# Kernel optimization log

Measured on AMD Instinct MI355X. Metric: run time of the kernel, lower is better.

## Reference

```python
import jax, jax.numpy as jnp
import numpy as np
from jax import lax

DIM = 512
DIM_KEY = 128


def _conv3x3_s2(x, w):
    # x: [N, C, H, W], w: [O, I, 3, 3]; stride-2, VALID (matches nn.Conv2d(dim, dim, 3, stride=2))
    return lax.conv_general_dilated(
        x, w, window_strides=(2, 2), padding='VALID',
        dimension_numbers=('NCHW', 'OIHW', 'NCHW'))


def setup_inputs() -> dict:
    key = jax.random.key(0)
    k1, k2, k3, k4, k5 = jax.random.split(key, 5)
    b, k, n, H, W = 8, 5, 5, 41, 41
    return {
        'img_query': jax.random.normal(k1, (b, DIM, H, W), dtype=jnp.float32),
        'img_supports': jax.random.normal(k2, (b, k, n, DIM, H, W), dtype=jnp.float32),
        'w_qk': jax.random.normal(k3, (DIM_KEY, DIM), dtype=jnp.float32) * 0.02,
        'w_v': jax.random.normal(k4, (DIM_KEY, DIM), dtype=jnp.float32) * 0.02,
        'w_ms': jax.random.normal(k5, (DIM, DIM, 3, 3), dtype=jnp.float32) * 0.02,
    }


def reference(img_query, img_supports, w_qk, w_v, w_ms):
    scale = DIM_KEY ** -0.5
    b, k, n = img_supports.shape[:3]

    # backbone `model` treated as identity; then multi-scale extracter (3x3 s2 conv)
    query_repr = _conv3x3_s2(img_query, w_ms)              # [b, c, h, w]
    h, w = query_repr.shape[-2:]
    supports = img_supports.reshape(b * k * n, DIM, *img_supports.shape[-2:])
    supports_repr = _conv3x3_s2(supports, w_ms)            # [bkn, c, h, w]

    # 1x1 convs as channel contractions
    query_q = jnp.einsum('bchw,dc->bdhw', query_repr, w_qk)
    query_v = jnp.einsum('bchw,dc->bdhw', query_repr, w_v)
    supports_k = jnp.einsum('schw,dc->sdhw', supports_repr, w_qk).reshape(b, k, n, DIM_KEY, h, w)
    supports_v = jnp.einsum('schw,dc->sdhw', supports_repr, w_v).reshape(b, k, n, DIM_KEY, h, w)

    # many-to-many cross attention over (n, i, j)
    sim = jnp.einsum('bchw,bkncij->bkhwnij', query_q, supports_k) * scale
    attn = jax.nn.softmax(sim.reshape(b, k, h, w, n * h * w), axis=-1)
    attn = attn.reshape(b, k, h, w, n, h, w)
    out = jnp.einsum('bkhwnij,bkncij->bkchw', attn, supports_v)

    out = out.reshape(b, k, -1)                     # [b, k, c*h*w]
    qv = query_v.reshape(b, 1, -1)                  # [b, 1, c*h*w]
    euclidean_dist = jnp.sum((qv - out) ** 2, axis=-1) / (h * w)
    return -euclidean_dist                          # [b, k]
```

## Files before the change

kernel.cpp:

```cpp
#include <hip/hip_runtime.h>

#define DIMC   512
#define HWIN   1681
#define WIN_   41
#define HWOUT  400
#define COUT   256
#define KD     4608
#define NIMG   208
#define NPAIR  40
#define NJ     2000

typedef __bf16 bf16;
typedef __bf16 bf16x4 __attribute__((ext_vector_type(4)));
typedef __bf16 bf16x8 __attribute__((ext_vector_type(8)));
typedef float  f32x16 __attribute__((ext_vector_type(16)));

#define OFF_WB   0ull
#define OFF_F    2359296ull
#define OFF_VT   44957696ull
#define OFF_DIST 65437696ull
#define OFF_R    65437952ull
#define WS_NEED  (OFF_R + 358039552ull)

__device__ __forceinline__ void gl2lds16(const void* g, void* l) {
  __builtin_amdgcn_global_load_lds((const __attribute__((address_space(1))) unsigned int*)g,
                                   (__attribute__((address_space(3))) unsigned int*)l,
                                   16, 0, 0);
}

__global__ __launch_bounds__(256) void k_wcomb(const float* __restrict__ wqk,
                                               const float* __restrict__ wv,
                                               const float* __restrict__ wms,
                                               bf16* __restrict__ Wb) {
  __shared__ float As[64][33];
  __shared__ float Bs[32][65];
  const int tid = threadIdx.x;
  const int bp = blockIdx.x, bn = blockIdx.y;
  const int tx = tid & 15, ty = tid >> 4;
  float acc[4][4] = {};
  for (int ko = 0; ko < 512; ko += 32) {
#pragma unroll
    for (int i = 0; i < 8; ++i) {
      int idx = tid + i * 256;
      int r = idx >> 5, c = idx & 31;
      int row = bn * 64 + r;
      As[r][c] = (row < 128) ? wqk[row * 512 + ko + c] : wv[(row - 128) * 512 + ko + c];
    }
#pragma unroll
    for (int i = 0; i < 8; ++i) {
      int idx = tid + i * 256;
      int r = idx >> 6, c = idx & 63;
      Bs[r][c] = wms[(size_t)(ko + r) * KD + bp * 64 + c];
    }
    __syncthreads();
#pragma unroll
    for (int kk = 0; kk < 32; ++kk) {
      float av[4], bv[4];
#pragma unroll
      for (int i = 0; i < 4; ++i) av[i] = As[ty * 4 + i][kk];
#pragma unroll
      for (int j = 0; j < 4; ++j) bv[j] = Bs[kk][tx * 4 + j];
#pragma unroll
      for (int i = 0; i < 4; ++i)
#pragma unroll
        for (int j = 0; j < 4; ++j) acc[i][j] += av[i] * bv[j];
    }
    __syncthreads();
  }
#pragma unroll
  for (int i = 0; i < 4; ++i)
#pragma unroll
    for (int j = 0; j < 4; ++j) {
      int n = bn * 64 + ty * 4 + i;
      int p = bp * 64 + tx * 4 + j;
      int c = p / 9, t = p - c * 9;
      Wb[(size_t)n * KD + t * DIMC + c] = (bf16)acc[i][j];
    }
}

__global__ __launch_bounds__(256) void k_repack(const float* __restrict__ q,
                                                const float* __restrict__ s,
                                                bf16* __restrict__ R) {
  __shared__ bf16 Ls[64][65];
  const int tid = threadIdx.x;
  const int bx = blockIdx.x, by = blockIdx.y, img = blockIdx.z;
  const float* src = (img < 8) ? (q + (size_t)img * DIMC * HWIN)
                               : (s + (size_t)(img - 8) * DIMC * HWIN);
  const int x0 = bx * 64, c0 = by * 64;
#pragma unroll
  for (int i = 0; i < 16; ++i) {
    int idx = i * 256 + tid;
    int r = idx >> 6, cx = idx & 63;
    int xx = x0 + cx;
    if (xx < HWIN) Ls[r][cx] = (bf16)src[(size_t)(c0 + r) * HWIN + xx];
  }
  __syncthreads();
#pragma unroll
  for (int i = 0; i < 4; ++i) {
    int idx = i * 256 + tid;
    int prow = idx >> 4, cq = idx & 15;
    int xx = x0 + prow;
    if (xx < HWIN) {
      bf16x4 v;
      v[0] = Ls[cq * 4 + 0][prow];
      v[1] = Ls[cq * 4 + 1][prow];
      v[2] = Ls[cq * 4 + 2][prow];
      v[3] = Ls[cq * 4 + 3][prow];
      *(bf16x4*)(R + ((size_t)img * HWIN + xx) * DIMC + c0 + cq * 4) = v;
    }
  }
}

__global__ __launch_bounds__(256) void k_conv(const bf16* __restrict__ R,
                                              const bf16* __restrict__ Wb,
                                              bf16* __restrict__ F) {
  __shared__ __align__(16) bf16 As[96 * 64];
  __shared__ __align__(16) bf16 Bs[256 * 64];
  const int tid = threadIdx.x;
  const int lane = tid & 63, wave = tid >> 6;
  const int mt = blockIdx.x, img = blockIdx.y;

  int aY[3], aX[3];
  unsigned aG[3];
#pragma unroll
  for (int i = 0; i < 3; ++i) {
    int issue = wave * 3 + i;
    int m = issue * 8 + (lane >> 3);
    int g = (lane & 7) ^ (m & 7);
    int pm = mt * 96 + m;
    if (pm >= HWOUT) pm = 0;
    int y = pm / 20, x = pm - y * 20;
    aY[i] = 2 * y; aX[i] = 2 * x; aG[i] = (unsigned)g * 8;
  }
  unsigned bOfs[8];
#pragma unroll
  for (int i = 0; i < 8; ++i) {
    int ib = wave * 8 + i;
    int n = ib * 8 + (lane >> 3);
    int g = (lane & 7) ^ (n & 7);
    bOfs[i] = (unsigned)n * KD + (unsigned)g * 8;
  }
  const size_t imgbase = (size_t)img * HWIN * DIMC;

  f32x16 acc[3][2];
#pragma unroll
  for (int mi = 0; mi < 3; ++mi)
#pragma unroll
    for (int ni = 0; ni < 2; ++ni)
#pragma unroll
      for (int r = 0; r < 16; ++r) acc[mi][ni][r] = 0.f;

  for (int t = 0; t < 9; ++t) {
    const int dy = t / 3, dx = t - dy * 3;
    for (int cc = 0; cc < 8; ++cc) {
      const int c0 = cc * 64;
#pragma unroll
      for (int i = 0; i < 3; ++i) {
        int issue = wave * 3 + i;
        unsigned off = (unsigned)(((aY[i] + dy) * WIN_ + (aX[i] + dx)) * DIMC + c0) + aG[i];
        gl2lds16(R + imgbase + off, (char*)As + issue * 1024);
      }
#pragma unroll
      for (int i = 0; i < 8; ++i) {
        int ib = wave * 8 + i;
        gl2lds16(Wb + bOfs[i] + (unsigned)(t * DIMC + c0), (char*)Bs + ib * 1024);
      }
      __syncthreads();
      const int mr = lane & 31;
#pragma unroll
      for (int kq = 0; kq < 4; ++kq) {
        const int chunk = kq * 2 + (lane >> 5);
        bf16x8 a[3], b[2];
#pragma unroll
        for (int mi = 0; mi < 3; ++mi) {
          int m = mi * 32 + mr;
          int slot = chunk ^ (m & 7);
          a[mi] = *(const bf16x8*)((const char*)As + m * 128 + slot * 16);
        }
#pragma unroll
        for (int ni = 0; ni < 2; ++ni) {
          int n = wave * 64 + ni * 32 + mr;
          int slot = chunk ^ (n & 7);
          b[ni] = *(const bf16x8*)((const char*)Bs + n * 128 + slot * 16);
        }
#pragma unroll
        for (int mi = 0; mi < 3; ++mi)
#pragma unroll
          for (int ni = 0; ni < 2; ++ni)
            acc[mi][ni] = __builtin_amdgcn_mfma_f32_32x32x16_bf16(a[mi], b[ni], acc[mi][ni], 0, 0, 0);
      }
      __syncthreads();
    }
  }
  const int col = lane & 31, hi = lane >> 5;
#pragma unroll
  for (int mi = 0; mi < 3; ++mi)
#pragma unroll
    for (int ni = 0; ni < 2; ++ni)
#pragma unroll
      for (int r = 0; r < 16; ++r) {
        int row = (r & 3) + 8 * (r >> 2) + 4 * hi;
        int pix = mt * 96 + mi * 32 + row;
        if (pix < HWOUT) {
          int ch = wave * 64 + ni * 32 + col;
          F[((size_t)img * HWOUT + pix) * COUT + ch] = (bf16)acc[mi][ni][r];
        }
      }
}

__global__ __launch_bounds__(256) void k_sim(const bf16* __restrict__ F,
                                             float* __restrict__ S) {
  __shared__ __align__(16) bf16 As[96 * 64];
  __shared__ __align__(16) bf16 Bs[256 * 64];
  const int tid = threadIdx.x, lane = tid & 63, wave = tid >> 6;
  const int mt = blockIdx.x, nt = blockIdx.y, pair = blockIdx.z;
  const int b = pair / 5, kidx = pair - b * 5;
  const int simg = 8 + b * 25 + kidx * 5;

  unsigned aBase[3];
#pragma unroll
  for (int i = 0; i < 3; ++i) {
    int issue = wave * 3 + i;
    int m = issue * 8 + (lane >> 3);
    int g = (lane & 7) ^ (m & 7);
    int pm = mt * 96 + m;
    if (pm >= HWOUT) pm = 0;
    aBase[i] = (unsigned)((b * HWOUT + pm) * COUT) + (unsigned)g * 8;
  }
  unsigned bBase[8];
#pragma unroll
  for (int i = 0; i < 8; ++i) {
    int ib = wave * 8 + i;
    int r = ib * 8 + (lane >> 3);
    int g = (lane & 7) ^ (r & 7);
    int jj = nt * 256 + r;
    if (jj >= NJ) jj = 0;
    int nimg = jj / HWOUT, ip = jj - nimg * HWOUT;
    bBase[i] = (unsigned)(((simg + nimg) * HWOUT + ip) * COUT) + (unsigned)g * 8;
  }

  f32x16 acc[3][2];
#pragma unroll
  for (int mi = 0; mi < 3; ++mi)
#pragma unroll
    for (int ni = 0; ni < 2; ++ni)
#pragma unroll
      for (int r = 0; r < 16; ++r) acc[mi][ni][r] = 0.f;

  for (int ks = 0; ks < 2; ++ks) {
    const int c0 = ks * 64;
#pragma unroll
    for (int i = 0; i < 3; ++i)
      gl2lds16(F + aBase[i] + c0, (char*)As + (wave * 3 + i) * 1024);
#pragma unroll
    for (int i = 0; i < 8; ++i)
      gl2lds16(F + bBase[i] + c0, (char*)Bs + (wave * 8 + i) * 1024);
    __syncthreads();
    const int mr = lane & 31;
#pragma unroll
    for (int kq = 0; kq < 4; ++kq) {
      const int chunk = kq * 2 + (lane >> 5);
      bf16x8 a[3], b[2];
#pragma unroll
      for (int mi = 0; mi < 3; ++mi) {
        int m = mi * 32 + mr;
        int slot = chunk ^ (m & 7);
        a[mi] = *(const bf16x8*)((const char*)As + m * 128 + slot * 16);
      }
#pragma unroll
      for (int ni = 0; ni < 2; ++ni) {
        int n = wave * 64 + ni * 32 + mr;
        int slot = chunk ^ (n & 7);
        b[ni] = *(const bf16x8*)((const char*)Bs + n * 128 + slot * 16);
      }
#pragma unroll
      for (int mi = 0; mi < 3; ++mi)
#pragma unroll
        for (int ni = 0; ni < 2; ++ni)
          acc[mi][ni] = __builtin_amdgcn_mfma_f32_32x32x16_bf16(a[mi], b[ni], acc[mi][ni], 0, 0, 0);
    }
    __syncthreads();
  }
  const float scale = 0.08838834764831845f;
  const int col = lane & 31, hi = lane >> 5;
#pragma unroll
  for (int mi = 0; mi < 3; ++mi)
#pragma unroll
    for (int ni = 0; ni < 2; ++ni)
#pragma unroll
      for (int r = 0; r < 16; ++r) {
        int row = (r & 3) + 8 * (r >> 2) + 4 * hi;
        int pix = mt * 96 + mi * 32 + row;
        int j = nt * 256 + wave * 64 + ni * 32 + col;
        if (pix < HWOUT && j < NJ)
          S[((size_t)pair * HWOUT + pix) * NJ + j] = acc[mi][ni][r] * scale;
      }
}

__global__ __launch_bounds__(256) void k_softmax(float* __restrict__ S) {
  const int row = blockIdx.x;
  const int tid = threadIdx.x;
  const int lane = tid & 63, wave = tid >> 6;
  float* rp = S + (size_t)row * NJ;
  float v[8];
  float mx = -1e30f;
#pragma unroll
  for (int i = 0; i < 8; ++i) {
    int idx = tid + i * 256;
    v[i] = (idx < NJ) ? rp[idx] : -1e30f;
    mx = fmaxf(mx, v[i]);
  }
  for (int off = 32; off > 0; off >>= 1) mx = fmaxf(mx, __shfl_xor(mx, off));
  __shared__ float sred[4];
  if (lane == 0) sred[wave] = mx;
  __syncthreads();
  mx = fmaxf(fmaxf(sred[0], sred[1]), fmaxf(sred[2], sred[3]));
  __syncthreads();
  float sum = 0.f;
#pragma unroll
  for (int i = 0; i < 8; ++i) {
    v[i] = __expf(v[i] - mx);
    sum += v[i];
  }
  for (int off = 32; off > 0; off >>= 1) sum += __shfl_xor(sum, off);
  if (lane == 0) sred[wave] = sum;
  __syncthreads();
  sum = sred[0] + sred[1] + sred[2] + sred[3];
  const float inv = 1.0f / sum;
  bf16* op = (bf16*)rp;
#pragma unroll
  for (int i = 0; i < 8; ++i) {
    int idx = tid + i * 256;
    if (idx < NJ) op[idx] = (bf16)(v[i] * inv);
  }
}

__global__ __launch_bounds__(256) void k_vt(const bf16* __restrict__ F,
                                            bf16* __restrict__ VT) {
  __shared__ bf16 Ls[64][132];
  const int tid = threadIdx.x;
  const int pt = blockIdx.x, n = blockIdx.y, pair = blockIdx.z;
  const int b = pair / 5, kidx = pair - b * 5;
  const int img = 8 + b * 25 + kidx * 5 + n;
#pragma unroll
  for (int i = 0; i < 8; ++i) {
    int idx = i * 256 + tid;
    int r = idx >> 5, cq = idx & 31;
    int ip = pt * 64 + r;
    if (ip < HWOUT) {
      bf16x4 t = *(const bf16x4*)(F + ((size_t)img * HWOUT + ip) * COUT + 128 + cq * 4);
      *(bf16x4*)(&Ls[r][cq * 4]) = t;
    }
  }
  __syncthreads();
#pragma unroll
  for (int i = 0; i < 8; ++i) {
    int idx = i * 256 + tid;
    int c = idx >> 4, iq = idx & 15;
    int ipb = pt * 64 + iq * 4;
    if (ipb + 3 < HWOUT) {
      bf16x4 v;
      v[0] = Ls[iq * 4 + 0][c];
      v[1] = Ls[iq * 4 + 1][c];
      v[2] = Ls[iq * 4 + 2][c];
      v[3] = Ls[iq * 4 + 3][c];
      *(bf16x4*)(VT + ((size_t)pair * 128 + c) * NJ + n * HWOUT + ipb) = v;
    }
  }
}

__global__ __launch_bounds__(256) void k_out(const char* __restrict__ Pbytes,
                                             const bf16* __restrict__ VT,
                                             const bf16* __restrict__ F,
                                             float* __restrict__ dist) {
  __shared__ __align__(16) bf16 As[96 * 128];
  __shared__ __align__(16) bf16 Bs[128 * 128];
  const int tid = threadIdx.x, lane = tid & 63, wave = tid >> 6;
  const int mt = blockIdx.x, pair = blockIdx.y;
  const int b = pair / 5;

  unsigned aByte[6]; int aGv[6];
#pragma unroll
  for (int i = 0; i < 6; ++i) {
    int issue = wave * 6 + i;
    int m = issue * 4 + (lane >> 4);
    int s_ = lane & 15;
    int g = s_ ^ (m & 7);
    int pm = mt * 96 + m;
    if (pm >= HWOUT) pm = 0;
    aByte[i] = (unsigned)((pair * HWOUT + pm) * 8000) + (unsigned)g * 16;
    aGv[i] = g;
  }
  unsigned bElem[8]; int bGv[8];
#pragma unroll
  for (int i = 0; i < 8; ++i) {
    int issue = wave * 8 + i;
    int c = issue * 4 + (lane >> 4);
    int s_ = lane & 15;
    int g = s_ ^ (c & 7);
    bElem[i] = (unsigned)((pair * 128 + c) * NJ) + (unsigned)g * 8;
    bGv[i] = g;
  }

  f32x16 acc[3];
#pragma unroll
  for (int mi = 0; mi < 3; ++mi)
#pragma unroll
    for (int r = 0; r < 16; ++r) acc[mi][r] = 0.f;

  const int mr = lane & 31;
  for (int step = 0; step < 16; ++step) {
    const int k0 = step * 128;
    const int nch = (step < 15) ? 16 : 10;
#pragma unroll
    for (int i = 0; i < 6; ++i) {
      if (aGv[i] < nch)
        gl2lds16(Pbytes + aByte[i] + k0 * 2, (char*)As + (wave * 6 + i) * 1024);
    }
#pragma unroll
    for (int i = 0; i < 8; ++i) {
      if (bGv[i] < nch)
        gl2lds16(VT + bElem[i] + k0, (char*)Bs + (wave * 8 + i) * 1024);
    }
    __syncthreads();
    auto body = [&](int kq) {
      const int chunk = kq * 2 + (lane >> 5);
      bf16x8 a[3], bb;
#pragma unroll
      for (int mi = 0; mi < 3; ++mi) {
        int m = mi * 32 + mr;
        int slot = chunk ^ (m & 7);
        a[mi] = *(const bf16x8*)((const char*)As + m * 256 + slot * 16);
      }
      {
        int n = wave * 32 + mr;
        int slot = chunk ^ (n & 7);
        bb = *(const bf16x8*)((const char*)Bs + n * 256 + slot * 16);
      }
#pragma unroll
      for (int mi = 0; mi < 3; ++mi)
        acc[mi] = __builtin_amdgcn_mfma_f32_32x32x16_bf16(a[mi], bb, acc[mi], 0, 0, 0);
    };
    if (step < 15) {
#pragma unroll
      for (int kq = 0; kq < 8; ++kq) body(kq);
    } else {
#pragma unroll
      for (int kq = 0; kq < 5; ++kq) body(kq);
    }
    __syncthreads();
  }

  const int col = lane & 31, hi = lane >> 5;
  float psum = 0.f;
#pragma unroll
  for (int mi = 0; mi < 3; ++mi)
#pragma unroll
    for (int r = 0; r < 16; ++r) {
      int row = (r & 3) + 8 * (r >> 2) + 4 * hi;
      int pix = mt * 96 + mi * 32 + row;
      if (pix < HWOUT) {
        int c = wave * 32 + col;
        float qv = (float)F[((size_t)b * HWOUT + pix) * COUT + 128 + c];
        float d = qv - acc[mi][r];
        psum += d * d;
      }
    }
  for (int off = 32; off > 0; off >>= 1) psum += __shfl_down(psum, off);
  __shared__ float ws4[4];
  if (lane == 0) ws4[wave] = psum;
  __syncthreads();
  if (tid == 0) atomicAdd(dist + pair, ws4[0] + ws4[1] + ws4[2] + ws4[3]);
}

__global__ void k_final(const float* __restrict__ dist, float* __restrict__ out) {
  int i = threadIdx.x;
  if (i < NPAIR) out[i] = -dist[i] * (1.0f / HWOUT);
}

extern "C" void kernel_launch(void* const* d_in, const int* in_sizes, int n_in,
                              void* d_out, int out_size, void* d_ws, size_t ws_size,
                              hipStream_t stream) {
  (void)in_sizes; (void)n_in; (void)out_size;
  if (ws_size < WS_NEED) return;

  const float* img_q = (const float*)d_in[0];
  const float* img_s = (const float*)d_in[1];
  const float* w_qk  = (const float*)d_in[2];
  const float* w_v   = (const float*)d_in[3];
  const float* w_ms  = (const float*)d_in[4];

  char* ws = (char*)d_ws;
  bf16*  Wb   = (bf16*)(ws + OFF_WB);
  bf16*  F    = (bf16*)(ws + OFF_F);
  bf16*  VT   = (bf16*)(ws + OFF_VT);
  float* dist = (float*)(ws + OFF_DIST);
  bf16*  R    = (bf16*)(ws + OFF_R);
  float* S    = (float*)(ws + OFF_R);

  hipMemsetAsync(dist, 0, NPAIR * sizeof(float), stream);
  k_wcomb  <<<dim3(72, 4),      256, 0, stream>>>(w_qk, w_v, w_ms, Wb);
  k_repack <<<dim3(27, 8, 208), 256, 0, stream>>>(img_q, img_s, R);
  k_conv   <<<dim3(5, 208),     256, 0, stream>>>(R, Wb, F);
  k_sim    <<<dim3(5, 8, 40),   256, 0, stream>>>(F, S);
  k_softmax<<<dim3(16000),      256, 0, stream>>>(S);
  k_vt     <<<dim3(7, 5, 40),   256, 0, stream>>>(F, VT);
  k_out    <<<dim3(5, 40),      256, 0, stream>>>((const char*)S, VT, F, dist);
  k_final  <<<1, 64,             0, stream>>>(dist, (float*)d_out);
}
```

Measured before the change: 1.460 ms.

## Flatten conv GEMM M across images with 128-row tiles to remove padding

The conv GEMM now treats all images' output pixels as one contiguous M dimension and tiles it in 128-row blocks across a 1D grid. Previously each image got padded 96-row tiles, which wasted compute. Larger M tiles also improve reuse of the weight tile loaded into LDS per k-step. The cost is more accumulator registers and LDS per block, plus a launch bound asking for two blocks per CU, which may constrain register allocation.

```diff
diff --git a/kernel.cpp b/kernel.cpp
--- a/kernel.cpp
+++ b/kernel.cpp
@@ -9,6 +9,7 @@
 #define NIMG   208
 #define NPAIR  40
 #define NJ     2000
+#define MTOT   83200
 
 typedef __bf16 bf16;
 typedef __bf16 bf16x4 __attribute__((ext_vector_type(4)));
@@ -111,26 +112,25 @@
   }
 }
 
-__global__ __launch_bounds__(256) void k_conv(const bf16* __restrict__ R,
-                                              const bf16* __restrict__ Wb,
-                                              bf16* __restrict__ F) {
-  __shared__ __align__(16) bf16 As[96 * 64];
+__global__ __launch_bounds__(256, 2) void k_conv(const bf16* __restrict__ R,
+                                                 const bf16* __restrict__ Wb,
+                                                 bf16* __restrict__ F) {
+  __shared__ __align__(16) bf16 As[128 * 64];
   __shared__ __align__(16) bf16 Bs[256 * 64];
   const int tid = threadIdx.x;
   const int lane = tid & 63, wave = tid >> 6;
-  const int mt = blockIdx.x, img = blockIdx.y;
-
-  int aY[3], aX[3];
-  unsigned aG[3];
-#pragma unroll
-  for (int i = 0; i < 3; ++i) {
-    int issue = wave * 3 + i;
+  const int blk = blockIdx.x;
+
+  unsigned aPix[4];
+#pragma unroll
+  for (int i = 0; i < 4; ++i) {
+    int issue = wave * 4 + i;
     int m = issue * 8 + (lane >> 3);
     int g = (lane & 7) ^ (m & 7);
-    int pm = mt * 96 + m;
-    if (pm >= HWOUT) pm = 0;
-    int y = pm / 20, x = pm - y * 20;
-    aY[i] = 2 * y; aX[i] = 2 * x; aG[i] = (unsigned)g * 8;
+    int gm = blk * 128 + m;
+    int img = gm / 400, p = gm - img * 400;
+    int oy = p / 20, ox = p - oy * 20;
+    aPix[i] = (unsigned)((img * HWIN + (2 * oy) * WIN_ + 2 * ox) * DIMC) + (unsigned)g * 8;
   }
   unsigned bOfs[8];
 #pragma unroll
@@ -140,11 +140,10 @@
     int g = (lane & 7) ^ (n & 7);
     bOfs[i] = (unsigned)n * KD + (unsigned)g * 8;
   }
-  const size_t imgbase = (size_t)img * HWIN * DIMC;
-
-  f32x16 acc[3][2];
-#pragma unroll
-  for (int mi = 0; mi < 3; ++mi)
+
+  f32x16 acc[4][2];
+#pragma unroll
+  for (int mi = 0; mi < 4; ++mi)
 #pragma unroll
     for (int ni = 0; ni < 2; ++ni)
 #pragma unroll
@@ -152,27 +151,27 @@
 
   for (int t = 0; t < 9; ++t) {
     const int dy = t / 3, dx = t - dy * 3;
+    const unsigned tapoff = (unsigned)((dy * WIN_ + dx) * DIMC);
     for (int cc = 0; cc < 8; ++cc) {
-      const int c0 = cc * 64;
-#pragma unroll
-      for (int i = 0; i < 3; ++i) {
-        int issue = wave * 3 + i;
-        unsigned off = (unsigned)(((aY[i] + dy) * WIN_ + (aX[i] + dx)) * DIMC + c0) + aG[i];
-        gl2lds16(R + imgbase + off, (char*)As + issue * 1024);
+      const unsigned c0 = (unsigned)(cc * 64);
+#pragma unroll
+      for (int i = 0; i < 4; ++i) {
+        int issue = wave * 4 + i;
+        gl2lds16(R + aPix[i] + tapoff + c0, (char*)As + issue * 1024);
       }
 #pragma unroll
       for (int i = 0; i < 8; ++i) {
         int ib = wave * 8 + i;
-        gl2lds16(Wb + bOfs[i] + (unsigned)(t * DIMC + c0), (char*)Bs + ib * 1024);
+        gl2lds16(Wb + bOfs[i] + (unsigned)(t * DIMC) + c0, (char*)Bs + ib * 1024);
       }
       __syncthreads();
       const int mr = lane & 31;
 #pragma unroll
       for (int kq = 0; kq < 4; ++kq) {
         const int chunk = kq * 2 + (lane >> 5);
-        bf16x8 a[3], b[2];
-#pragma unroll
-        for (int mi = 0; mi < 3; ++mi) {
+        bf16x8 a[4], b[2];
+#pragma unroll
+        for (int mi = 0; mi < 4; ++mi) {
           int m = mi * 32 + mr;
           int slot = chunk ^ (m & 7);
           a[mi] = *(const bf16x8*)((const char*)As + m * 128 + slot * 16);
@@ -184,7 +183,7 @@
           b[ni] = *(const bf16x8*)((const char*)Bs + n * 128 + slot * 16);
         }
 #pragma unroll
-        for (int mi = 0; mi < 3; ++mi)
+        for (int mi = 0; mi < 4; ++mi)
 #pragma unroll
           for (int ni = 0; ni < 2; ++ni)
             acc[mi][ni] = __builtin_amdgcn_mfma_f32_32x32x16_bf16(a[mi], b[ni], acc[mi][ni], 0, 0, 0);
@@ -194,17 +193,15 @@
   }
   const int col = lane & 31, hi = lane >> 5;
 #pragma unroll
-  for (int mi = 0; mi < 3; ++mi)
+  for (int mi = 0; mi < 4; ++mi)
 #pragma unroll
     for (int ni = 0; ni < 2; ++ni)
 #pragma unroll
       for (int r = 0; r < 16; ++r) {
         int row = (r & 3) + 8 * (r >> 2) + 4 * hi;
-        int pix = mt * 96 + mi * 32 + row;
-        if (pix < HWOUT) {
-          int ch = wave * 64 + ni * 32 + col;
-          F[((size_t)img * HWOUT + pix) * COUT + ch] = (bf16)acc[mi][ni][r];
-        }
+        int gm = blk * 128 + mi * 32 + row;
+        int ch = wave * 64 + ni * 32 + col;
+        F[(size_t)gm * COUT + ch] = (bf16)acc[mi][ni][r];
       }
 }
 
@@ -501,7 +498,7 @@
   hipMemsetAsync(dist, 0, NPAIR * sizeof(float), stream);
   k_wcomb  <<<dim3(72, 4),      256, 0, stream>>>(w_qk, w_v, w_ms, Wb);
   k_repack <<<dim3(27, 8, 208), 256, 0, stream>>>(img_q, img_s, R);
-  k_conv   <<<dim3(5, 208),     256, 0, stream>>>(R, Wb, F);
+  k_conv   <<<dim3(650),        256, 0, stream>>>(R, Wb, F);
   k_sim    <<<dim3(5, 8, 40),   256, 0, stream>>>(F, S);
   k_softmax<<<dim3(16000),      256, 0, stream>>>(S);
   k_vt     <<<dim3(7, 5, 40),   256, 0, stream>>>(F, VT);
```

Result: faster. 1.402 ms (-4.0%).
